# Kernel tuning notes

Hardware: AMD Instinct MI355X
Metric: run time of the kernel (lower is better)

Reference implementation:

```python
import jax, jax.numpy as jnp
import numpy as np

B, S, D = 2, 2048, 4096
NH, NKV, HD = 32, 8, 128
NREP = NH // NKV
ROPE_THETA = 10000.0


def setup_inputs() -> dict:
    key = jax.random.key(0)
    k1, k2, k3, k4, k5 = jax.random.split(key, 5)
    x = jax.random.normal(k1, (B, S, D), jnp.float32)
    wq = jax.random.normal(k2, (NH * HD, D), jnp.float32) * 0.02
    wk = jax.random.normal(k3, (NKV * HD, D), jnp.float32) * 0.02
    wv = jax.random.normal(k4, (NKV * HD, D), jnp.float32) * 0.02
    wo = jax.random.normal(k5, (D, NH * HD), jnp.float32) * 0.02
    inv_freq = 1.0 / (ROPE_THETA ** (np.arange(0, HD, 2, dtype=np.float64) / HD))
    ang = np.outer(np.arange(S, dtype=np.float64), inv_freq)  # [S, HD/2]
    return {
        'x': x, 'start_pos': 0,
        'freqs_cos': jnp.asarray(np.cos(ang), jnp.float32),
        'freqs_sin': jnp.asarray(np.sin(ang), jnp.float32),
        'wq': wq, 'wk': wk, 'wv': wv, 'wo': wo,
    }


def _apply_rope(x, cos, sin):
    # x: [B, S, H, HD]; cos/sin: [S, HD/2]. Matches torch view_as_complex on
    # interleaved (even, odd) feature pairs: (xr + i*xi) * (cos + i*sin).
    xr = x[..., 0::2]
    xi = x[..., 1::2]
    c = cos[None, :, None, :]
    s = sin[None, :, None, :]
    out_r = xr * c - xi * s
    out_i = xr * s + xi * c
    return jnp.stack([out_r, out_i], axis=-1).reshape(x.shape)


def reference(x, start_pos, freqs_cos, freqs_sin, wq, wk, wv, wo):
    b, s, _ = x.shape
    xq = (x @ wq.T).reshape(b, s, NH, HD)
    xk = (x @ wk.T).reshape(b, s, NKV, HD)
    xv = (x @ wv.T).reshape(b, s, NKV, HD)
    # Source applies RoPE to K and V (not Q) -- reproduced faithfully.
    xk = _apply_rope(xk, freqs_cos, freqs_sin)
    xv = _apply_rope(xv, freqs_cos, freqs_sin)
    # start_pos == 0 prefill: cache slice [:, :start_pos+s] == freshly written xk/xv.
    # repeat_kv: head h_out = h_kv * NREP + rep  ==  jnp.repeat along head axis.
    keys = jnp.repeat(xk, NREP, axis=2)    # [B, S, NH, HD]
    values = jnp.repeat(xv, NREP, axis=2)  # [B, S, NH, HD]
    scale = 1.0 / jnp.sqrt(jnp.asarray(HD, x.dtype))
    scores = jnp.einsum('bqhd,bkhd->bhqk', xq, keys) * scale  # [B, NH, S, S]
    probs = jax.nn.softmax(scores, axis=-1)  # NOTE: no causal mask in source
    out = jnp.einsum('bhqk,bkhd->bqhd', probs, values).reshape(b, s, NH * HD)
    return out @ wo.T
```

## Files before the change

### kernel.cpp

```cpp
#include <hip/hip_runtime.h>
#include <hip/hip_bf16.h>


typedef short bf16x8 __attribute__((ext_vector_type(8)));
typedef float f32x4 __attribute__((ext_vector_type(4)));

__device__ __forceinline__ void load16(const void* g, void* l) {
  __builtin_amdgcn_global_load_lds(
      (const __attribute__((address_space(1))) void*)g,
      (__attribute__((address_space(3))) void*)l, 16, 0, 0);
}

__device__ __forceinline__ f32x4 mfma16(bf16x8 a, bf16x8 b, f32x4 c) {
  return __builtin_amdgcn_mfma_f32_16x16x32_bf16(a, b, c, 0, 0, 0);
}

__device__ __forceinline__ unsigned short f2b(float f) {
  union { float f; unsigned int u; } v; v.f = f;
  unsigned int u = v.u;
  return (unsigned short)((u + 0x7fffu + ((u >> 16) & 1u)) >> 16);
}
__device__ __forceinline__ float b2f(unsigned short u) {
  union { unsigned int u; float f; } v; v.u = ((unsigned int)u) << 16;
  return v.f;
}
__device__ __forceinline__ unsigned short f2b_fast(float f) {
  __hip_bfloat16 h = __float2bfloat16(f);
  return *reinterpret_cast<unsigned short*>(&h);
}

#define QSCALE (0.08838834764831845f * 1.4426950408889634f)

__global__ __launch_bounds__(256) void cvt_f32_bf16(
    const float* __restrict__ in, unsigned short* __restrict__ out, int n4) {
  int idx = blockIdx.x * 256 + threadIdx.x;
  int stride = gridDim.x * 256;
  for (int i = idx; i < n4; i += stride) {
    float4 v = reinterpret_cast<const float4*>(in)[i];
    ushort4 o;
    o.x = f2b(v.x); o.y = f2b(v.y); o.z = f2b(v.z); o.w = f2b(v.w);
    reinterpret_cast<ushort4*>(out)[i] = o;
  }
}

template <typename OutT>
__global__ __launch_bounds__(512, 2) void gemm256(
    const unsigned short* __restrict__ A, const unsigned short* __restrict__ Bw,
    OutT* __restrict__ C, int M, int N, int K, int sbl) {
  extern __shared__ char smem[];
  const int tid = threadIdx.x;
  const int lane = tid & 63;
  const int w = tid >> 6;
  const int lr = lane & 15, lg = lane >> 4;
  const int wr = w >> 2, wc = w & 3;

  const int nbn = N >> 8;
  const int bid = blockIdx.x, nwg = gridDim.x;
  const int swz = (bid & 7) * (nwg >> 3) + (bid >> 3);
  const int bm = swz / nbn, bn = swz % nbn;

  const unsigned short* Ag = A + (size_t)bm * 256 * K;
  const unsigned short* Bg = Bw + (size_t)bn * 256 * K;

  int srow[4], skhw[4], sdst[4];
#pragma unroll
  for (int j = 0; j < 4; ++j) {
    const int c = tid + j * 512;
    srow[j] = c >> 3;
    skhw[j] = ((c & 7) ^ ((c >> 3) & 7)) << 3;
    sdst[j] = ((tid & ~63) << 4) + j * 8192;
  }

  f32x4 acc[8][4];
#pragma unroll
  for (int m = 0; m < 8; ++m)
#pragma unroll
    for (int n = 0; n < 4; ++n) acc[m][n] = (f32x4){0.f, 0.f, 0.f, 0.f};

#define STAGEA4(tt)                                                           \
  {                                                                           \
    char* d = smem + (((tt)&1) * 65536);                                      \
    _Pragma("unroll") for (int j = 0; j < 4; ++j)                             \
        load16(Ag + (size_t)srow[j] * K + ((tt) << 6) + skhw[j], d + sdst[j]);\
  }
#define STAGEB4(tt)                                                           \
  {                                                                           \
    char* d = smem + (((tt)&1) * 65536) + 32768;                              \
    _Pragma("unroll") for (int j = 0; j < 4; ++j)                             \
        load16(Bg + (size_t)srow[j] * K + ((tt) << 6) + skhw[j], d + sdst[j]);\
  }

  STAGEB4(0);
  STAGEA4(0);

  const int NT = K >> 6;
  const int rx = (lr & 7) << 4;
  const int aRow0 = (wr * 128 + lr) * 128;
  const int bRow0 = (wc * 64 + lr) * 128;
  const int col0 = (lg * 16) ^ rx;
  const int col1 = (64 + lg * 16) ^ rx;

  bf16x8 aR[4][2], bR[4][2];

  for (int t = 0; t < NT; ++t) {
    const char* bufA = smem + (t & 1) * 65536;
    const char* bufB = bufA + 32768;
    const bool more = (t + 1) < NT;

    asm volatile("s_waitcnt vmcnt(0)" ::: "memory");
    __builtin_amdgcn_s_barrier();

#pragma unroll
    for (int mf = 0; mf < 4; ++mf) {
      aR[mf][0] = *(const bf16x8*)(bufA + aRow0 + mf * 2048 + col0);
      aR[mf][1] = *(const bf16x8*)(bufA + aRow0 + mf * 2048 + col1);
    }
#pragma unroll
    for (int nf = 0; nf < 2; ++nf) {
      bR[nf][0] = *(const bf16x8*)(bufB + bRow0 + nf * 2048 + col0);
      bR[nf][1] = *(const bf16x8*)(bufB + bRow0 + nf * 2048 + col1);
    }
    if (more) STAGEB4(t + 1);
    asm volatile("s_waitcnt lgkmcnt(8)" ::: "memory");
    __builtin_amdgcn_s_barrier();
    asm volatile("s_waitcnt lgkmcnt(0)" ::: "memory");
    __builtin_amdgcn_sched_barrier(0);
    __builtin_amdgcn_s_setprio(1);
#pragma unroll
    for (int mf = 0; mf < 4; ++mf)
#pragma unroll
      for (int nf = 0; nf < 2; ++nf) {
        acc[mf][nf] = mfma16(aR[mf][0], bR[nf][0], acc[mf][nf]);
        acc[mf][nf] = mfma16(aR[mf][1], bR[nf][1], acc[mf][nf]);
      }
    __builtin_amdgcn_s_setprio(0);
    __builtin_amdgcn_s_barrier();

#pragma unroll
    for (int nf = 2; nf < 4; ++nf) {
      bR[nf][0] = *(const bf16x8*)(bufB + bRow0 + nf * 2048 + col0);
      bR[nf][1] = *(const bf16x8*)(bufB + bRow0 + nf * 2048 + col1);
    }
    if (more) STAGEA4(t + 1);
    __builtin_amdgcn_s_barrier();
    asm volatile("s_waitcnt lgkmcnt(0)" ::: "memory");
    __builtin_amdgcn_sched_barrier(0);
    __builtin_amdgcn_s_setprio(1);
#pragma unroll
    for (int mf = 0; mf < 4; ++mf)
#pragma unroll
      for (int nf = 2; nf < 4; ++nf) {
        acc[mf][nf] = mfma16(aR[mf][0], bR[nf][0], acc[mf][nf]);
        acc[mf][nf] = mfma16(aR[mf][1], bR[nf][1], acc[mf][nf]);
      }
    __builtin_amdgcn_s_setprio(0);
    __builtin_amdgcn_s_barrier();

#pragma unroll
    for (int mf = 0; mf < 4; ++mf) {
      aR[mf][0] = *(const bf16x8*)(bufA + aRow0 + (4 + mf) * 2048 + col0);
      aR[mf][1] = *(const bf16x8*)(bufA + aRow0 + (4 + mf) * 2048 + col1);
    }
    __builtin_amdgcn_s_barrier();
    asm volatile("s_waitcnt lgkmcnt(0)" ::: "memory");
    __builtin_amdgcn_sched_barrier(0);
    __builtin_amdgcn_s_setprio(1);
#pragma unroll
    for (int mf = 0; mf < 4; ++mf)
#pragma unroll
      for (int nf = 0; nf < 2; ++nf) {
        acc[4 + mf][nf] = mfma16(aR[mf][0], bR[nf][0], acc[4 + mf][nf]);
        acc[4 + mf][nf] = mfma16(aR[mf][1], bR[nf][1], acc[4 + mf][nf]);
      }
    __builtin_amdgcn_s_setprio(0);
    __builtin_amdgcn_s_barrier();

    __builtin_amdgcn_s_setprio(1);
#pragma unroll
    for (int mf = 0; mf < 4; ++mf)
#pragma unroll
      for (int nf = 2; nf < 4; ++nf) {
        acc[4 + mf][nf] = mfma16(aR[mf][0], bR[nf][0], acc[4 + mf][nf]);
        acc[4 + mf][nf] = mfma16(aR[mf][1], bR[nf][1], acc[4 + mf][nf]);
      }
    __builtin_amdgcn_s_setprio(0);
  }
#undef STAGEA4
#undef STAGEB4

  const float cscale = (bn < sbl) ? QSCALE : 1.0f;
#pragma unroll
  for (int mf = 0; mf < 8; ++mf)
#pragma unroll
    for (int nf = 0; nf < 4; ++nf)
#pragma unroll
      for (int r = 0; r < 4; ++r) {
        int rowc = bm * 256 + wr * 128 + mf * 16 + lg * 4 + r;
        int colc = bn * 256 + wc * 64 + nf * 16 + lr;
        float v = acc[mf][nf][r] * cscale;
        if constexpr (sizeof(OutT) == 2)
          C[(size_t)rowc * N + colc] = (OutT)f2b(v);
        else
          C[(size_t)rowc * N + colc] = v;
      }
}

__global__ __launch_bounds__(256) void rope_kv(
    const unsigned short* __restrict__ XQKV,
    const float* __restrict__ fc, const float* __restrict__ fs,
    unsigned short* __restrict__ Kr, unsigned short* __restrict__ Vt) {
  __shared__ unsigned short Vl[128][66];
  const int t = threadIdx.x;
  const int bid = blockIdx.x;
  const int stile = bid & 31, bkv = bid >> 5;
  const int b = bkv >> 3, kvh = bkv & 7;
  const int s0 = stile * 64;
  const int l = t & 63;
  const int jrow = t >> 6;

  for (int j = 0; j < 16; ++j) {
    int s = s0 + j * 4 + jrow;
    ushort2 v = *(const ushort2*)(XQKV + (size_t)(b * 2048 + s) * 6144 + 4096 +
                                  kvh * 128 + 2 * l);
    float c = fc[s * 64 + l], sn = fs[s * 64 + l];
    float xr = b2f(v.x), xi = b2f(v.y);
    ushort2 o;
    o.x = f2b(xr * c - xi * sn);
    o.y = f2b(xr * sn + xi * c);
    *(ushort2*)(Kr + ((size_t)bkv * 2048 + s) * 128 + 2 * l) = o;
  }
  for (int j = 0; j < 16; ++j) {
    int ss = j * 4 + jrow;
    int s = s0 + ss;
    ushort2 v = *(const ushort2*)(XQKV + (size_t)(b * 2048 + s) * 6144 + 5120 +
                                  kvh * 128 + 2 * l);
    float c = fc[s * 64 + l], sn = fs[s * 64 + l];
    float xr = b2f(v.x), xi = b2f(v.y);
    Vl[2 * l][ss] = f2b(xr * c - xi * sn);
    Vl[2 * l + 1][ss] = f2b(xr * sn + xi * c);
  }
  __syncthreads();
  const int d = t >> 1, half = t & 1;
  unsigned short* vdst = Vt + ((size_t)bkv * 128 + d) * 2048 + s0 + half * 32;
#pragma unroll
  for (int e = 0; e < 32; e += 4) {
    ushort4 pk;
    pk.x = Vl[d][half * 32 + e];
    pk.y = Vl[d][half * 32 + e + 1];
    pk.z = Vl[d][half * 32 + e + 2];
    pk.w = Vl[d][half * 32 + e + 3];
    *(ushort4*)(vdst + e) = pk;
  }
}

__global__ __launch_bounds__(256, 2) void attn_fwd(
    const unsigned short* __restrict__ XQ, const unsigned short* __restrict__ Kr,
    const unsigned short* __restrict__ Vt, unsigned short* __restrict__ AO) {
  extern __shared__ char smem[];
  char* Ksm = smem;
  char* Vsm = smem + 32768;
  unsigned short* Ps = (unsigned short*)(smem + 65536);
  const int t = threadIdx.x;
  const int lane = t & 63, w = t >> 6;
  const int lr = lane & 15, lg = lane >> 4;

  const int bid = blockIdx.x;
  const int nwg = gridDim.x;
  const int swz = (bid & 7) * (nwg >> 3) + (bid >> 3);
  const int qt = swz & 15;
  const int bh = swz >> 4;
  const int b = bh >> 5, h = bh & 31;
  const int bkv = b * 8 + (h >> 2);

  bf16x8 qf[2][4];
#pragma unroll
  for (int q2 = 0; q2 < 2; ++q2) {
    const unsigned short* qp =
        XQ + ((size_t)(b * 2048 + qt * 128 + w * 32 + q2 * 16 + lr)) * 6144 +
        h * 128 + lg * 8;
#pragma unroll
    for (int dc = 0; dc < 4; ++dc) qf[q2][dc] = *(const bf16x8*)(qp + dc * 32);
  }

  f32x4 acc[2][8];
#pragma unroll
  for (int q2 = 0; q2 < 2; ++q2)
#pragma unroll
    for (int i = 0; i < 8; ++i) acc[q2][i] = (f32x4){0.f, 0.f, 0.f, 0.f};
  float l_[2][4] = {{0.f, 0.f, 0.f, 0.f}, {0.f, 0.f, 0.f, 0.f}};

  const unsigned short* Kbase = Kr + (size_t)bkv * 2048 * 128;
  const unsigned short* Vbase = Vt + (size_t)bkv * 128 * 2048;

  int kK[4], dC[4], vD[4], vKc[4], dstb[4];
#pragma unroll
  for (int j = 0; j < 4; ++j) {
    const int c = t + j * 256;
    kK[j] = c & 63;  dC[j] = c >> 6;
    vD[j] = c & 127; vKc[j] = c >> 7;
    dstb[j] = (c & ~63) * 16;
  }

#define STAGE_KV(bufi, kt)                                                    \
  {                                                                           \
    char* kd = Ksm + (bufi)*16384;                                            \
    char* vd = Vsm + (bufi)*16384;                                            \
    _Pragma("unroll") for (int j = 0; j < 4; ++j) {                           \
      load16(Kbase + (size_t)((kt)*64 + kK[j]) * 128 + dC[j] * 8, kd + dstb[j]); \
      load16(Vbase + (size_t)vD[j] * 2048 + (kt)*64 + vKc[j] * 8, vd + dstb[j]); \
    }                                                                         \
  }

  STAGE_KV(0, 0);
  asm volatile("s_waitcnt vmcnt(0)" ::: "memory");
  __builtin_amdgcn_s_barrier();

  unsigned short* Pw = Ps + w * 2048;
  const int pbase = (lr >> 3) * 256 + (lr & 7);

  for (int kt = 0; kt < 32; ++kt) {
    const int cur = kt & 1;
    if (kt < 31) STAGE_KV(cur ^ 1, kt + 1);

    const char* Kc = Ksm + cur * 16384;
    const char* Vc = Vsm + cur * 16384;

#pragma unroll
    for (int nf = 0; nf < 4; ++nf) {
      f32x4 s0 = (f32x4){0.f, 0.f, 0.f, 0.f};
      f32x4 s1 = (f32x4){0.f, 0.f, 0.f, 0.f};
#pragma unroll
      for (int dc = 0; dc < 4; ++dc) {
        bf16x8 kf =
            *(const bf16x8*)(Kc + ((dc * 4 + lg) * 64 + nf * 16 + lr) * 16);
        s0 = mfma16(qf[0][dc], kf, s0);
        s1 = mfma16(qf[1][dc], kf, s1);
      }
      const int pb = pbase + nf * 512;
#pragma unroll
      for (int r = 0; r < 4; ++r) {
        float p0 = __builtin_amdgcn_exp2f(s0[r]);
        float p1 = __builtin_amdgcn_exp2f(s1[r]);
        l_[0][r] += p0;
        l_[1][r] += p1;
        Pw[pb + (lg * 4 + r) * 8] = f2b_fast(p0);
        Pw[pb + (16 + lg * 4 + r) * 8] = f2b_fast(p1);
      }
    }

#pragma unroll
    for (int ks = 0; ks < 2; ++ks) {
      bf16x8 pf0 = *(const bf16x8*)(Pw + (ks * 4 + lg) * 256 + lr * 8);
      bf16x8 pf1 = *(const bf16x8*)(Pw + (ks * 4 + lg) * 256 + (16 + lr) * 8);
#pragma unroll
      for (int dt = 0; dt < 8; ++dt) {
        bf16x8 vf =
            *(const bf16x8*)(Vc + ((ks * 4 + lg) * 128 + dt * 16 + lr) * 16);
        acc[0][dt] = mfma16(pf0, vf, acc[0][dt]);
        acc[1][dt] = mfma16(pf1, vf, acc[1][dt]);
      }
    }

    asm volatile("s_waitcnt vmcnt(0)" ::: "memory");
    __builtin_amdgcn_s_barrier();
  }
#undef STAGE_KV

#pragma unroll
  for (int q2 = 0; q2 < 2; ++q2)
#pragma unroll
    for (int r = 0; r < 4; ++r) {
#pragma unroll
      for (int o = 1; o < 16; o <<= 1) l_[q2][r] += __shfl_xor(l_[q2][r], o);
    }

#pragma unroll
  for (int q2 = 0; q2 < 2; ++q2)
#pragma unroll
    for (int r = 0; r < 4; ++r) {
      float inv = 1.f / l_[q2][r];
      size_t rowb =
          ((size_t)(b * 2048 + qt * 128 + w * 32 + q2 * 16 + lg * 4 + r)) * 4096 +
          h * 128;
#pragma unroll
      for (int dt = 0; dt < 8; ++dt)
        AO[rowb + dt * 16 + lr] = f2b_fast(acc[q2][dt][r] * inv);
    }
}

extern "C" void kernel_launch(void* const* d_in, const int* in_sizes, int n_in,
                              void* d_out, int out_size, void* d_ws, size_t ws_size,
                              hipStream_t stream) {
  const float* x  = (const float*)d_in[0];
  const float* fc = (const float*)d_in[2];
  const float* fs = (const float*)d_in[3];
  const float* wq = (const float*)d_in[4];
  const float* wk = (const float*)d_in[5];
  const float* wv = (const float*)d_in[6];
  const float* wo = (const float*)d_in[7];

  const size_t MB = 1024ull * 1024ull;
  char* ws = (char*)d_ws;
  unsigned short* Xb   = (unsigned short*)(ws);
  unsigned short* Wsc  = (unsigned short*)(ws + 32 * MB);
  unsigned short* Kr   = (unsigned short*)(ws);
  unsigned short* Vt   = (unsigned short*)(ws + 8 * MB);
  unsigned short* AO   = (unsigned short*)(ws + 80 * MB);
  unsigned short* XQKV = (unsigned short*)d_out;

  (void)hipFuncSetAttribute((const void*)gemm256<unsigned short>,
                            hipFuncAttributeMaxDynamicSharedMemorySize, 131072);
  (void)hipFuncSetAttribute((const void*)gemm256<float>,
                            hipFuncAttributeMaxDynamicSharedMemorySize, 131072);
  (void)hipFuncSetAttribute((const void*)attn_fwd,
                            hipFuncAttributeMaxDynamicSharedMemorySize, 81920);

  dim3 blk(256);
  dim3 blk512(512);
  cvt_f32_bf16<<<2048, blk, 0, stream>>>(x, Xb, (2 * 2048 * 4096) / 4);
  cvt_f32_bf16<<<2048, blk, 0, stream>>>(wq, Wsc, (4096 * 4096) / 4);
  cvt_f32_bf16<<<2048, blk, 0, stream>>>(wk, Wsc + 4096 * 4096, (1024 * 4096) / 4);
  cvt_f32_bf16<<<2048, blk, 0, stream>>>(wv, Wsc + 5120 * 4096, (1024 * 4096) / 4);
  gemm256<unsigned short><<<384, blk512, 131072, stream>>>(
      Xb, Wsc, XQKV, 4096, 6144, 4096, 16);
  rope_kv<<<512, blk, 0, stream>>>(XQKV, fc, fs, Kr, Vt);
  attn_fwd<<<1024, blk, 81920, stream>>>(XQKV, Kr, Vt, AO);
  cvt_f32_bf16<<<2048, blk, 0, stream>>>(wo, Wsc, (4096 * 4096) / 4);
  gemm256<float><<<256, blk512, 131072, stream>>>(
      AO, Wsc, (float*)d_out, 4096, 4096, 4096, 0);
}
```

Before: 563.2 us.

## Restructure GEMM LDS layout into K-half planes with finer-grained staged loads

Replaces the XOR-swizzled row-major LDS tile with a layout split into two K halves (32 elements each), with lane groups reading contiguous 16-byte chunks from separate 4 KB planes. Global-to-LDS staging is broken into four half-tile loads interleaved across the four MFMA phases, and vmcnt waits are relaxed to vmcnt(2) and vmcnt(4) so later loads stay in flight. The aim is fewer register fragments per phase and more overlap of global loads with MFMA work. The unswizzled plane layout may bring back LDS bank conflicts, and the extra barrier per iteration adds synchronisation.

```diff
diff --git a/kernel.cpp b/kernel.cpp
--- a/kernel.cpp
+++ b/kernel.cpp
@@ -62,14 +62,9 @@
   const unsigned short* Ag = A + (size_t)bm * 256 * K;
   const unsigned short* Bg = Bw + (size_t)bn * 256 * K;
 
-  int srow[4], skhw[4], sdst[4];
-#pragma unroll
-  for (int j = 0; j < 4; ++j) {
-    const int c = tid + j * 512;
-    srow[j] = c >> 3;
-    skhw[j] = ((c & 7) ^ ((c >> 3) & 7)) << 3;
-    sdst[j] = ((tid & ~63) << 4) + j * 8192;
-  }
+  const int row0 = tid & 255, kc0 = tid >> 8;
+  const int row1 = tid & 255, kc1 = (tid >> 8) + 2;
+  const int sdst = (tid & ~63) * 16;
 
   f32x4 acc[8][4];
 #pragma unroll
@@ -77,116 +72,107 @@
 #pragma unroll
     for (int n = 0; n < 4; ++n) acc[m][n] = (f32x4){0.f, 0.f, 0.f, 0.f};
 
-#define STAGEA4(tt)                                                           \
+#define STAGE_H(gptr, obase, hh, tt)                                          \
   {                                                                           \
-    char* d = smem + (((tt)&1) * 65536);                                      \
-    _Pragma("unroll") for (int j = 0; j < 4; ++j)                             \
-        load16(Ag + (size_t)srow[j] * K + ((tt) << 6) + skhw[j], d + sdst[j]);\
-  }
-#define STAGEB4(tt)                                                           \
-  {                                                                           \
-    char* d = smem + (((tt)&1) * 65536) + 32768;                              \
-    _Pragma("unroll") for (int j = 0; j < 4; ++j)                             \
-        load16(Bg + (size_t)srow[j] * K + ((tt) << 6) + skhw[j], d + sdst[j]);\
-  }
-
-  STAGEB4(0);
-  STAGEA4(0);
+    char* d = smem + (((tt)&1) * 65536) + (obase) + (hh)*16384;               \
+    load16(gptr + (size_t)row0 * K + ((tt) << 6) + (hh)*32 + kc0 * 8,         \
+           d + sdst);                                                         \
+    load16(gptr + (size_t)row1 * K + ((tt) << 6) + (hh)*32 + kc1 * 8,         \
+           d + sdst + 8192);                                                  \
+  }
+
+  STAGE_H(Ag, 0, 0, 0);
+  STAGE_H(Ag, 0, 1, 0);
+  STAGE_H(Bg, 32768, 0, 0);
+  STAGE_H(Bg, 32768, 1, 0);
 
   const int NT = K >> 6;
-  const int rx = (lr & 7) << 4;
-  const int aRow0 = (wr * 128 + lr) * 128;
-  const int bRow0 = (wc * 64 + lr) * 128;
-  const int col0 = (lg * 16) ^ rx;
-  const int col1 = (64 + lg * 16) ^ rx;
-
-  bf16x8 aR[4][2], bR[4][2];
+  const int aRowB = (wr * 128 + lr) * 16 + lg * 4096;
+  const int bRowB = (wc * 64 + lr) * 16 + lg * 4096;
+
+  bf16x8 aR[8], bR[4];
 
   for (int t = 0; t < NT; ++t) {
     const char* bufA = smem + (t & 1) * 65536;
     const char* bufB = bufA + 32768;
     const bool more = (t + 1) < NT;
 
-    asm volatile("s_waitcnt vmcnt(0)" ::: "memory");
-    __builtin_amdgcn_s_barrier();
-
-#pragma unroll
-    for (int mf = 0; mf < 4; ++mf) {
-      aR[mf][0] = *(const bf16x8*)(bufA + aRow0 + mf * 2048 + col0);
-      aR[mf][1] = *(const bf16x8*)(bufA + aRow0 + mf * 2048 + col1);
-    }
-#pragma unroll
-    for (int nf = 0; nf < 2; ++nf) {
-      bR[nf][0] = *(const bf16x8*)(bufB + bRow0 + nf * 2048 + col0);
-      bR[nf][1] = *(const bf16x8*)(bufB + bRow0 + nf * 2048 + col1);
-    }
-    if (more) STAGEB4(t + 1);
-    asm volatile("s_waitcnt lgkmcnt(8)" ::: "memory");
+    asm volatile("s_waitcnt vmcnt(2)" ::: "memory");
+    __builtin_amdgcn_s_barrier();
+#pragma unroll
+    for (int mf = 0; mf < 8; ++mf)
+      aR[mf] = *(const bf16x8*)(bufA + aRowB + mf * 256);
+#pragma unroll
+    for (int nf = 0; nf < 2; ++nf)
+      bR[nf] = *(const bf16x8*)(bufB + bRowB + nf * 256);
+    if (more) STAGE_H(Ag, 0, 0, t + 1);
     __builtin_amdgcn_s_barrier();
     asm volatile("s_waitcnt lgkmcnt(0)" ::: "memory");
     __builtin_amdgcn_sched_barrier(0);
     __builtin_amdgcn_s_setprio(1);
 #pragma unroll
-    for (int mf = 0; mf < 4; ++mf)
-#pragma unroll
-      for (int nf = 0; nf < 2; ++nf) {
-        acc[mf][nf] = mfma16(aR[mf][0], bR[nf][0], acc[mf][nf]);
-        acc[mf][nf] = mfma16(aR[mf][1], bR[nf][1], acc[mf][nf]);
-      }
+    for (int mf = 0; mf < 8; ++mf)
+#pragma unroll
+      for (int nf = 0; nf < 2; ++nf)
+        acc[mf][nf] = mfma16(aR[mf], bR[nf], acc[mf][nf]);
     __builtin_amdgcn_s_setprio(0);
     __builtin_amdgcn_s_barrier();
 
 #pragma unroll
-    for (int nf = 2; nf < 4; ++nf) {
-      bR[nf][0] = *(const bf16x8*)(bufB + bRow0 + nf * 2048 + col0);
-      bR[nf][1] = *(const bf16x8*)(bufB + bRow0 + nf * 2048 + col1);
-    }
-    if (more) STAGEA4(t + 1);
+    for (int nf = 2; nf < 4; ++nf)
+      bR[nf] = *(const bf16x8*)(bufB + bRowB + nf * 256);
+    if (more) STAGE_H(Ag, 0, 1, t + 1);
     __builtin_amdgcn_s_barrier();
     asm volatile("s_waitcnt lgkmcnt(0)" ::: "memory");
     __builtin_amdgcn_sched_barrier(0);
     __builtin_amdgcn_s_setprio(1);
 #pragma unroll
-    for (int mf = 0; mf < 4; ++mf)
-#pragma unroll
-      for (int nf = 2; nf < 4; ++nf) {
-        acc[mf][nf] = mfma16(aR[mf][0], bR[nf][0], acc[mf][nf]);
-        acc[mf][nf] = mfma16(aR[mf][1], bR[nf][1], acc[mf][nf]);
-      }
+    for (int mf = 0; mf < 8; ++mf)
+#pragma unroll
+      for (int nf = 2; nf < 4; ++nf)
+        acc[mf][nf] = mfma16(aR[mf], bR[nf], acc[mf][nf]);
     __builtin_amdgcn_s_setprio(0);
     __builtin_amdgcn_s_barrier();
 
-#pragma unroll
-    for (int mf = 0; mf < 4; ++mf) {
-      aR[mf][0] = *(const bf16x8*)(bufA + aRow0 + (4 + mf) * 2048 + col0);
-      aR[mf][1] = *(const bf16x8*)(bufA + aRow0 + (4 + mf) * 2048 + col1);
-    }
+    if (more) { asm volatile("s_waitcnt vmcnt(4)" ::: "memory"); }
+    else      { asm volatile("s_waitcnt vmcnt(0)" ::: "memory"); }
+    __builtin_amdgcn_s_barrier();
+#pragma unroll
+    for (int mf = 0; mf < 8; ++mf)
+      aR[mf] = *(const bf16x8*)(bufA + 16384 + aRowB + mf * 256);
+#pragma unroll
+    for (int nf = 0; nf < 2; ++nf)
+      bR[nf] = *(const bf16x8*)(bufB + 16384 + bRowB + nf * 256);
+    if (more) STAGE_H(Bg, 32768, 0, t + 1);
     __builtin_amdgcn_s_barrier();
     asm volatile("s_waitcnt lgkmcnt(0)" ::: "memory");
     __builtin_amdgcn_sched_barrier(0);
     __builtin_amdgcn_s_setprio(1);
 #pragma unroll
-    for (int mf = 0; mf < 4; ++mf)
-#pragma unroll
-      for (int nf = 0; nf < 2; ++nf) {
-        acc[4 + mf][nf] = mfma16(aR[mf][0], bR[nf][0], acc[4 + mf][nf]);
-        acc[4 + mf][nf] = mfma16(aR[mf][1], bR[nf][1], acc[4 + mf][nf]);
-      }
+    for (int mf = 0; mf < 8; ++mf)
+#pragma unroll
+      for (int nf = 0; nf < 2; ++nf)
+        acc[mf][nf] = mfma16(aR[mf], bR[nf], acc[mf][nf]);
     __builtin_amdgcn_s_setprio(0);
     __builtin_amdgcn_s_barrier();
 
+#pragma unroll
+    for (int nf = 2; nf < 4; ++nf)
+      bR[nf] = *(const bf16x8*)(bufB + 16384 + bRowB + nf * 256);
+    if (more) STAGE_H(Bg, 32768, 1, t + 1);
+    __builtin_amdgcn_s_barrier();
+    asm volatile("s_waitcnt lgkmcnt(0)" ::: "memory");
+    __builtin_amdgcn_sched_barrier(0);
     __builtin_amdgcn_s_setprio(1);
 #pragma unroll
-    for (int mf = 0; mf < 4; ++mf)
-#pragma unroll
-      for (int nf = 2; nf < 4; ++nf) {
-        acc[4 + mf][nf] = mfma16(aR[mf][0], bR[nf][0], acc[4 + mf][nf]);
-        acc[4 + mf][nf] = mfma16(aR[mf][1], bR[nf][1], acc[4 + mf][nf]);
-      }
+    for (int mf = 0; mf < 8; ++mf)
+#pragma unroll
+      for (int nf = 2; nf < 4; ++nf)
+        acc[mf][nf] = mfma16(aR[mf], bR[nf], acc[mf][nf]);
     __builtin_amdgcn_s_setprio(0);
-  }
-#undef STAGEA4
-#undef STAGEB4
+    __builtin_amdgcn_s_barrier();
+  }
+#undef STAGE_H
 
   const float cscale = (bn < sbl) ? QSCALE : 1.0f;
 #pragma unroll
```

After: 702.8 us. 1.25x slower.

## Enlarge attention query tile to 256 rows with 32-key K/V steps

Applied to the files above, without the earlier changes.

Each attention workgroup now handles 256 query rows (64 per wave) instead of 128, and steps through keys in chunks of 32 instead of 64. The kernel launches half as many workgroups and uses less LDS for K/V and P staging. The goal is to reuse each staged K/V tile across twice as many query rows, halving global K/V traffic, while keeping LDS small. The cost is more accumulator and Q-fragment registers per thread, which can lower occupancy or cause spills, plus twice as many loop iterations and barriers over the keys.

```diff
diff --git a/kernel.cpp b/kernel.cpp
--- a/kernel.cpp
+++ b/kernel.cpp
@@ -258,8 +258,8 @@
     const unsigned short* __restrict__ Vt, unsigned short* __restrict__ AO) {
   extern __shared__ char smem[];
   char* Ksm = smem;
-  char* Vsm = smem + 32768;
-  unsigned short* Ps = (unsigned short*)(smem + 65536);
+  char* Vsm = smem + 16384;
+  unsigned short* Ps = (unsigned short*)(smem + 32768);
   const int t = threadIdx.x;
   const int lane = t & 63, w = t >> 6;
   const int lr = lane & 15, lg = lane >> 4;
@@ -267,48 +267,51 @@
   const int bid = blockIdx.x;
   const int nwg = gridDim.x;
   const int swz = (bid & 7) * (nwg >> 3) + (bid >> 3);
-  const int qt = swz & 15;
-  const int bh = swz >> 4;
+  const int qt = swz & 7;
+  const int bh = swz >> 3;
   const int b = bh >> 5, h = bh & 31;
   const int bkv = b * 8 + (h >> 2);
 
-  bf16x8 qf[2][4];
-#pragma unroll
-  for (int q2 = 0; q2 < 2; ++q2) {
+  bf16x8 qf[4][4];
+#pragma unroll
+  for (int q4 = 0; q4 < 4; ++q4) {
     const unsigned short* qp =
-        XQ + ((size_t)(b * 2048 + qt * 128 + w * 32 + q2 * 16 + lr)) * 6144 +
+        XQ + ((size_t)(b * 2048 + qt * 256 + w * 64 + q4 * 16 + lr)) * 6144 +
         h * 128 + lg * 8;
 #pragma unroll
-    for (int dc = 0; dc < 4; ++dc) qf[q2][dc] = *(const bf16x8*)(qp + dc * 32);
-  }
-
-  f32x4 acc[2][8];
-#pragma unroll
-  for (int q2 = 0; q2 < 2; ++q2)
-#pragma unroll
-    for (int i = 0; i < 8; ++i) acc[q2][i] = (f32x4){0.f, 0.f, 0.f, 0.f};
-  float l_[2][4] = {{0.f, 0.f, 0.f, 0.f}, {0.f, 0.f, 0.f, 0.f}};
+    for (int dc = 0; dc < 4; ++dc) qf[q4][dc] = *(const bf16x8*)(qp + dc * 32);
+  }
+
+  f32x4 acc[4][8];
+#pragma unroll
+  for (int q4 = 0; q4 < 4; ++q4)
+#pragma unroll
+    for (int i = 0; i < 8; ++i) acc[q4][i] = (f32x4){0.f, 0.f, 0.f, 0.f};
+  float l_[4][4];
+#pragma unroll
+  for (int q4 = 0; q4 < 4; ++q4)
+#pragma unroll
+    for (int r = 0; r < 4; ++r) l_[q4][r] = 0.f;
 
   const unsigned short* Kbase = Kr + (size_t)bkv * 2048 * 128;
   const unsigned short* Vbase = Vt + (size_t)bkv * 128 * 2048;
 
-  int kK[4], dC[4], vD[4], vKc[4], dstb[4];
-#pragma unroll
-  for (int j = 0; j < 4; ++j) {
-    const int c = t + j * 256;
-    kK[j] = c & 63;  dC[j] = c >> 6;
-    vD[j] = c & 127; vKc[j] = c >> 7;
-    dstb[j] = (c & ~63) * 16;
-  }
-
-#define STAGE_KV(bufi, kt)                                                    \
-  {                                                                           \
-    char* kd = Ksm + (bufi)*16384;                                            \
-    char* vd = Vsm + (bufi)*16384;                                            \
-    _Pragma("unroll") for (int j = 0; j < 4; ++j) {                           \
-      load16(Kbase + (size_t)((kt)*64 + kK[j]) * 128 + dC[j] * 8, kd + dstb[j]); \
-      load16(Vbase + (size_t)vD[j] * 2048 + (kt)*64 + vKc[j] * 8, vd + dstb[j]); \
-    }                                                                         \
+  const int c0 = t, c1 = t + 256;
+  const int kK0 = c0 & 31, dC0 = c0 >> 5;
+  const int kK1 = c1 & 31, dC1 = c1 >> 5;
+  const int vD0 = c0 & 127, vKc0 = c0 >> 7;
+  const int vD1 = c1 & 127, vKc1 = c1 >> 7;
+  const int dstb0 = (c0 & ~63) * 16;
+  const int dstb1 = (c1 & ~63) * 16;
+
+#define STAGE_KV(bufi, kt)                                                     \
+  {                                                                            \
+    char* kd = Ksm + (bufi)*8192;                                              \
+    char* vd = Vsm + (bufi)*8192;                                              \
+    load16(Kbase + (size_t)((kt)*32 + kK0) * 128 + dC0 * 8, kd + dstb0);       \
+    load16(Kbase + (size_t)((kt)*32 + kK1) * 128 + dC1 * 8, kd + dstb1);       \
+    load16(Vbase + (size_t)vD0 * 2048 + (kt)*32 + vKc0 * 8, vd + dstb0);       \
+    load16(Vbase + (size_t)vD1 * 2048 + (kt)*32 + vKc1 * 8, vd + dstb1);       \
   }
 
   STAGE_KV(0, 0);
@@ -316,49 +319,48 @@
   __builtin_amdgcn_s_barrier();
 
   unsigned short* Pw = Ps + w * 2048;
-  const int pbase = (lr >> 3) * 256 + (lr & 7);
-
-  for (int kt = 0; kt < 32; ++kt) {
+  const int pbase = (lr >> 3) * 512 + (lr & 7);
+
+  for (int kt = 0; kt < 64; ++kt) {
     const int cur = kt & 1;
-    if (kt < 31) STAGE_KV(cur ^ 1, kt + 1);
-
-    const char* Kc = Ksm + cur * 16384;
-    const char* Vc = Vsm + cur * 16384;
-
-#pragma unroll
-    for (int nf = 0; nf < 4; ++nf) {
-      f32x4 s0 = (f32x4){0.f, 0.f, 0.f, 0.f};
-      f32x4 s1 = (f32x4){0.f, 0.f, 0.f, 0.f};
+    if (kt < 63) STAGE_KV(cur ^ 1, kt + 1);
+
+    const char* Kc = Ksm + cur * 8192;
+    const char* Vc = Vsm + cur * 8192;
+
+#pragma unroll
+    for (int nf = 0; nf < 2; ++nf) {
+      f32x4 s[4];
+#pragma unroll
+      for (int q4 = 0; q4 < 4; ++q4) s[q4] = (f32x4){0.f, 0.f, 0.f, 0.f};
 #pragma unroll
       for (int dc = 0; dc < 4; ++dc) {
         bf16x8 kf =
-            *(const bf16x8*)(Kc + ((dc * 4 + lg) * 64 + nf * 16 + lr) * 16);
-        s0 = mfma16(qf[0][dc], kf, s0);
-        s1 = mfma16(qf[1][dc], kf, s1);
-      }
-      const int pb = pbase + nf * 512;
-#pragma unroll
-      for (int r = 0; r < 4; ++r) {
-        float p0 = __builtin_amdgcn_exp2f(s0[r]);
-        float p1 = __builtin_amdgcn_exp2f(s1[r]);
-        l_[0][r] += p0;
-        l_[1][r] += p1;
-        Pw[pb + (lg * 4 + r) * 8] = f2b_fast(p0);
-        Pw[pb + (16 + lg * 4 + r) * 8] = f2b_fast(p1);
-      }
-    }
-
-#pragma unroll
-    for (int ks = 0; ks < 2; ++ks) {
-      bf16x8 pf0 = *(const bf16x8*)(Pw + (ks * 4 + lg) * 256 + lr * 8);
-      bf16x8 pf1 = *(const bf16x8*)(Pw + (ks * 4 + lg) * 256 + (16 + lr) * 8);
-#pragma unroll
-      for (int dt = 0; dt < 8; ++dt) {
-        bf16x8 vf =
-            *(const bf16x8*)(Vc + ((ks * 4 + lg) * 128 + dt * 16 + lr) * 16);
-        acc[0][dt] = mfma16(pf0, vf, acc[0][dt]);
-        acc[1][dt] = mfma16(pf1, vf, acc[1][dt]);
-      }
+            *(const bf16x8*)(Kc + ((dc * 4 + lg) * 32 + nf * 16 + lr) * 16);
+#pragma unroll
+        for (int q4 = 0; q4 < 4; ++q4) s[q4] = mfma16(qf[q4][dc], kf, s[q4]);
+      }
+      const int pb = pbase + nf * 1024;
+#pragma unroll
+      for (int q4 = 0; q4 < 4; ++q4)
+#pragma unroll
+        for (int r = 0; r < 4; ++r) {
+          float p = __builtin_amdgcn_exp2f(s[q4][r]);
+          l_[q4][r] += p;
+          Pw[pb + (q4 * 16 + lg * 4 + r) * 8] = f2b_fast(p);
+        }
+    }
+
+    bf16x8 pf[4];
+#pragma unroll
+    for (int q4 = 0; q4 < 4; ++q4)
+      pf[q4] = *(const bf16x8*)(Pw + lg * 512 + (q4 * 16 + lr) * 8);
+#pragma unroll
+    for (int dt = 0; dt < 8; ++dt) {
+      bf16x8 vf = *(const bf16x8*)(Vc + (lg * 128 + dt * 16 + lr) * 16);
+#pragma unroll
+      for (int q4 = 0; q4 < 4; ++q4)
+        acc[q4][dt] = mfma16(pf[q4], vf, acc[q4][dt]);
     }
 
     asm volatile("s_waitcnt vmcnt(0)" ::: "memory");
@@ -367,24 +369,24 @@
 #undef STAGE_KV
 
 #pragma unroll
-  for (int q2 = 0; q2 < 2; ++q2)
+  for (int q4 = 0; q4 < 4; ++q4)
 #pragma unroll
     for (int r = 0; r < 4; ++r) {
 #pragma unroll
-      for (int o = 1; o < 16; o <<= 1) l_[q2][r] += __shfl_xor(l_[q2][r], o);
-    }
-
-#pragma unroll
-  for (int q2 = 0; q2 < 2; ++q2)
+      for (int o = 1; o < 16; o <<= 1) l_[q4][r] += __shfl_xor(l_[q4][r], o);
+    }
+
+#pragma unroll
+  for (int q4 = 0; q4 < 4; ++q4)
 #pragma unroll
     for (int r = 0; r < 4; ++r) {
-      float inv = 1.f / l_[q2][r];
+      float inv = 1.f / l_[q4][r];
       size_t rowb =
-          ((size_t)(b * 2048 + qt * 128 + w * 32 + q2 * 16 + lg * 4 + r)) * 4096 +
+          ((size_t)(b * 2048 + qt * 256 + w * 64 + q4 * 16 + lg * 4 + r)) * 4096 +
           h * 128;
 #pragma unroll
       for (int dt = 0; dt < 8; ++dt)
-        AO[rowb + dt * 16 + lr] = f2b_fast(acc[q2][dt][r] * inv);
+        AO[rowb + dt * 16 + lr] = f2b_fast(acc[q4][dt][r] * inv);
     }
 }
 
@@ -413,7 +415,7 @@
   (void)hipFuncSetAttribute((const void*)gemm256<float>,
                             hipFuncAttributeMaxDynamicSharedMemorySize, 131072);
   (void)hipFuncSetAttribute((const void*)attn_fwd,
-                            hipFuncAttributeMaxDynamicSharedMemorySize, 81920);
+                            hipFuncAttributeMaxDynamicSharedMemorySize, 49152);
 
   dim3 blk(256);
   dim3 blk512(512);
@@ -424,7 +426,7 @@
   gemm256<unsigned short><<<384, blk512, 131072, stream>>>(
       Xb, Wsc, XQKV, 4096, 6144, 4096, 16);
   rope_kv<<<512, blk, 0, stream>>>(XQKV, fc, fs, Kr, Vt);
-  attn_fwd<<<1024, blk, 81920, stream>>>(XQKV, Kr, Vt, AO);
+  attn_fwd<<<512, blk, 49152, stream>>>(XQKV, Kr, Vt, AO);
   cvt_f32_bf16<<<2048, blk, 0, stream>>>(wo, Wsc, (4096 * 4096) / 4);
   gemm256<float><<<256, blk512, 131072, stream>>>(
       AO, Wsc, (float*)d_out, 4096, 4096, 4096, 0);
```

Result: no change. 564.7 us (+0.3%).
